# Kernel optimization log

Measured on AMD Instinct MI355X. Metric: run time of the kernel, lower is better.

## Reference

```python
import jax, jax.numpy as jnp
import numpy as np

MARGIN = 0.3
IN_FEATURES = 128
NUM_CLASSES = 100
BATCH = 4096


def setup_inputs() -> dict:
    key = jax.random.key(0)
    k1, k2, k3, k4 = jax.random.split(key, 4)
    embeddings = jax.random.normal(k1, (BATCH, IN_FEATURES), dtype=jnp.float32)
    labels = jax.random.randint(k2, (BATCH,), 0, NUM_CLASSES, dtype=jnp.int64)
    # nn.Linear params (kaiming-uniform-ish scale)
    bound = 1.0 / np.sqrt(IN_FEATURES)
    fc_w = jax.random.uniform(k3, (NUM_CLASSES, IN_FEATURES), jnp.float32, -bound, bound)
    fc_b = jax.random.uniform(k4, (NUM_CLASSES,), jnp.float32, -bound, bound)
    return {"embeddings": embeddings, "labels": labels, "fc_w": fc_w, "fc_b": fc_b}


def _triplet_hard(emb, labels, margin):
    # pairwise squared euclidean distances: ||a||^2 + ||b||^2 - 2 a.b
    sq = jnp.sum(emb * emb, axis=1)  # [B]
    d2 = sq[:, None] + sq[None, :] - 2.0 * (emb @ emb.T)
    dist = jnp.sqrt(jnp.clip(d2, 1e-12))  # [B, B]
    same = labels[:, None] == labels[None, :]  # [B, B] (diag True, as in torch)
    neg_inf = jnp.float32(-jnp.inf)
    pos_inf = jnp.float32(jnp.inf)
    ap = jnp.max(jnp.where(same, dist, neg_inf), axis=1)  # hardest positive
    an = jnp.min(jnp.where(same, pos_inf, dist), axis=1)  # hardest negative
    # MarginRankingLoss(target=1): mean(relu(-(an - ap) + margin))
    return jnp.mean(jax.nn.relu(ap - an + margin))


def _cross_entropy(logits, labels):
    logp = jax.nn.log_softmax(logits, axis=-1)
    return -jnp.mean(jnp.take_along_axis(logp, labels[:, None], axis=1)[:, 0])


def reference(embeddings, labels, fc_w, fc_b):
    logits = embeddings @ fc_w.T + fc_b  # [B, C]
    triplet = _triplet_hard(embeddings, labels, MARGIN)
    ce = _cross_entropy(logits, labels)
    return triplet + ce
```

## Files before the change

### kernel.cpp

```cpp
#include <hip/hip_runtime.h>
#include <math.h>

#define BATCH 4096
#define DIM 128
#define NCLS 100
#define MARGIN 0.3f

typedef __attribute__((ext_vector_type(8))) short short8;
typedef __attribute__((ext_vector_type(4))) float f32x4;

__device__ __forceinline__ unsigned short f2bf(float f) {
    unsigned int u = __float_as_uint(f);
    unsigned int r = (u + 0x7FFFu + ((u >> 16) & 1u)) >> 16;
    return (unsigned short)r;
}
__device__ __forceinline__ float bf2f(unsigned short b) {
    return __uint_as_float(((unsigned int)b) << 16);
}

__global__ __launch_bounds__(256) void prep_kernel(
        const float* __restrict__ emb, const float* __restrict__ fcw,
        unsigned short* __restrict__ ebf, float* __restrict__ sq,
        unsigned short* __restrict__ wbf) {
    int bid = blockIdx.x, tid = threadIdx.x;
    if (bid < 256) {
        int wave = tid >> 6, lane = tid & 63;
        #pragma unroll
        for (int r = 0; r < 4; ++r) {
            int row = bid * 16 + wave * 4 + r;
            const float2* src = reinterpret_cast<const float2*>(emb + row * DIM);
            float2 xy = src[lane];
            unsigned short b0 = f2bf(xy.x), b1 = f2bf(xy.y);
            float y0 = bf2f(b0), y1 = bf2f(b1);
            reinterpret_cast<unsigned int*>(ebf + row * DIM)[lane] =
                ((unsigned int)b1 << 16) | (unsigned int)b0;
            float acc = y0 * y0 + y1 * y1;
            #pragma unroll
            for (int off = 1; off < 64; off <<= 1) acc += __shfl_xor(acc, off, 64);
            if (lane == 0) sq[row] = acc;
        }
    } else {
        int idx = (bid - 256) * 256 + tid;
        for (int k = idx; k < 112 * DIM; k += 512) {
            wbf[k] = (k < NCLS * DIM) ? f2bf(fcw[k]) : (unsigned short)0;
        }
    }
}

__global__ __launch_bounds__(256) void main_kernel(
        const unsigned short* __restrict__ ebf, const unsigned short* __restrict__ wbf,
        const float* __restrict__ sq, const int* __restrict__ labels,
        const float* __restrict__ fcb,
        float* __restrict__ appart, float* __restrict__ anpart,
        float* __restrict__ ce) {
    __shared__ float lg[16][128];
    int bid = blockIdx.x, tid = threadIdx.x;
    int wave = tid >> 6, lane = tid & 63;
    int lm = lane & 15, lq = lane >> 4;
    int koff = lq * 8;

    if (bid < 1024) {
        int rowgrp = bid >> 4, chunk = bid & 15;
        int rbase = rowgrp * 64 + wave * 16;
        int arow = rbase + lm;
        const unsigned short* apt = ebf + arow * DIM + koff;
        short8 a0 = *reinterpret_cast<const short8*>(apt);
        short8 a1 = *reinterpret_cast<const short8*>(apt + 32);
        short8 a2 = *reinterpret_cast<const short8*>(apt + 64);
        short8 a3 = *reinterpret_cast<const short8*>(apt + 96);

        int labr[4];
        #pragma unroll
        for (int r = 0; r < 4; ++r) labr[r] = labels[rbase + lq * 4 + r];

        float rmax[4] = {-INFINITY, -INFINITY, -INFINITY, -INFINITY};
        float rmin[4] = { INFINITY,  INFINITY,  INFINITY,  INFINITY};

        int cbase = chunk * 256;
        #pragma unroll 4
        for (int ct = 0; ct < 16; ++ct) {
            int col = cbase + ct * 16 + lm;
            const unsigned short* bp = ebf + col * DIM + koff;
            short8 b0 = *reinterpret_cast<const short8*>(bp);
            short8 b1 = *reinterpret_cast<const short8*>(bp + 32);
            short8 b2 = *reinterpret_cast<const short8*>(bp + 64);
            short8 b3 = *reinterpret_cast<const short8*>(bp + 96);
            f32x4 c = {0.f, 0.f, 0.f, 0.f};
            c = __builtin_amdgcn_mfma_f32_16x16x32_bf16(a0, b0, c, 0, 0, 0);
            c = __builtin_amdgcn_mfma_f32_16x16x32_bf16(a1, b1, c, 0, 0, 0);
            c = __builtin_amdgcn_mfma_f32_16x16x32_bf16(a2, b2, c, 0, 0, 0);
            c = __builtin_amdgcn_mfma_f32_16x16x32_bf16(a3, b3, c, 0, 0, 0);
            float sqc = sq[col];
            int lc = labels[col];
            #pragma unroll
            for (int r = 0; r < 4; ++r) {
                float v = fmaf(c[r], -2.0f, sqc);
                bool same = (lc == labr[r]);
                rmax[r] = same ? fmaxf(rmax[r], v) : rmax[r];
                rmin[r] = same ? rmin[r] : fminf(rmin[r], v);
            }
        }
        #pragma unroll
        for (int off = 1; off < 16; off <<= 1) {
            #pragma unroll
            for (int r = 0; r < 4; ++r) {
                rmax[r] = fmaxf(rmax[r], __shfl_xor(rmax[r], off, 64));
                rmin[r] = fminf(rmin[r], __shfl_xor(rmin[r], off, 64));
            }
        }
        if (lm == 0) {
            int row0 = rbase + lq * 4;
            #pragma unroll
            for (int r = 0; r < 4; ++r) {
                appart[(row0 + r) * 16 + chunk] = rmax[r];
                anpart[(row0 + r) * 16 + chunk] = rmin[r];
            }
        }
    } else {
        int R0 = (bid - 1024) * 16;
        lg[tid >> 4][112 + (tid & 15)] = -INFINITY;

        int arow = R0 + lm;
        const unsigned short* apt = ebf + arow * DIM + koff;
        short8 a0 = *reinterpret_cast<const short8*>(apt);
        short8 a1 = *reinterpret_cast<const short8*>(apt + 32);
        short8 a2 = *reinterpret_cast<const short8*>(apt + 64);
        short8 a3 = *reinterpret_cast<const short8*>(apt + 96);

        for (int t = wave * 2; t < 7 && t < wave * 2 + 2; ++t) {
            int cls = t * 16 + lm;
            const unsigned short* bp = wbf + cls * DIM + koff;
            short8 b0 = *reinterpret_cast<const short8*>(bp);
            short8 b1 = *reinterpret_cast<const short8*>(bp + 32);
            short8 b2 = *reinterpret_cast<const short8*>(bp + 64);
            short8 b3 = *reinterpret_cast<const short8*>(bp + 96);
            f32x4 c = {0.f, 0.f, 0.f, 0.f};
            c = __builtin_amdgcn_mfma_f32_16x16x32_bf16(a0, b0, c, 0, 0, 0);
            c = __builtin_amdgcn_mfma_f32_16x16x32_bf16(a1, b1, c, 0, 0, 0);
            c = __builtin_amdgcn_mfma_f32_16x16x32_bf16(a2, b2, c, 0, 0, 0);
            c = __builtin_amdgcn_mfma_f32_16x16x32_bf16(a3, b3, c, 0, 0, 0);
            float bias = (cls < NCLS) ? fcb[cls] : -INFINITY;
            #pragma unroll
            for (int r = 0; r < 4; ++r)
                lg[lq * 4 + r][t * 16 + lm] = c[r] + bias;
        }
        __syncthreads();
        #pragma unroll
        for (int i = 0; i < 4; ++i) {
            int r = wave * 4 + i;
            float x0 = lg[r][lane], x1 = lg[r][lane + 64];
            float m = fmaxf(x0, x1);
            #pragma unroll
            for (int off = 1; off < 64; off <<= 1) m = fmaxf(m, __shfl_xor(m, off, 64));
            float s = expf(x0 - m) + expf(x1 - m);
            #pragma unroll
            for (int off = 1; off < 64; off <<= 1) s += __shfl_xor(s, off, 64);
            if (lane == 0) {
                int lab = labels[R0 + r];
                ce[R0 + r] = (m + logf(s)) - lg[r][lab];
            }
        }
    }
}

__global__ __launch_bounds__(256) void final_kernel(
        const float* __restrict__ sq, const float* __restrict__ appart,
        const float* __restrict__ anpart, const float* __restrict__ ce,
        float* __restrict__ out) {
    __shared__ float red[256];
    int tid = threadIdx.x, bid = blockIdx.x;
    float acc = 0.f;
    #pragma unroll
    for (int rr = 0; rr < 2; ++rr) {
        int row = bid * 512 + rr * 256 + tid;
        const float4* ap = reinterpret_cast<const float4*>(appart + row * 16);
        const float4* an = reinterpret_cast<const float4*>(anpart + row * 16);
        float m = -INFINITY, n = INFINITY;
        #pragma unroll
        for (int p = 0; p < 4; ++p) {
            float4 a = ap[p];
            m = fmaxf(m, fmaxf(fmaxf(a.x, a.y), fmaxf(a.z, a.w)));
            float4 b = an[p];
            n = fminf(n, fminf(fminf(b.x, b.y), fminf(b.z, b.w)));
        }
        float api = sqrtf(fmaxf(sq[row] + m, 1e-12f));
        float ani = sqrtf(fmaxf(sq[row] + n, 1e-12f));
        acc += fmaxf(api - ani + MARGIN, 0.f) + ce[row];
    }
    red[tid] = acc;
    __syncthreads();
    for (int s = 128; s > 0; s >>= 1) {
        if (tid < s) red[tid] += red[tid + s];
        __syncthreads();
    }
    if (tid == 0) atomicAdd(out, red[0] * (1.0f / BATCH));
}

extern "C" void kernel_launch(void* const* d_in, const int* in_sizes, int n_in,
                              void* d_out, int out_size, void* d_ws, size_t ws_size,
                              hipStream_t stream) {
    const float* emb    = (const float*)d_in[0];
    const int*   labels = (const int*)  d_in[1];
    const float* fcw    = (const float*)d_in[2];
    const float* fcb    = (const float*)d_in[3];
    float* out = (float*)d_out;

    char* ws = (char*)d_ws;
    unsigned short* ebf = (unsigned short*)(ws);
    unsigned short* wbf = (unsigned short*)(ws + 1048576);
    float* sq     = (float*)(ws + 1081344);
    float* ce     = (float*)(ws + 1097728);
    float* appart = (float*)(ws + 1114112);
    float* anpart = (float*)(ws + 1376256);

    hipMemsetAsync(out, 0, sizeof(float), stream);
    prep_kernel<<<258, 256, 0, stream>>>(emb, fcw, ebf, sq, wbf);
    main_kernel<<<1280, 256, 0, stream>>>(ebf, wbf, sq, labels, fcb, appart, anpart, ce);
    final_kernel<<<8, 256, 0, stream>>>(sq, appart, anpart, ce, out);
}
```

Measured before the change: 109.2 us.

## Fuse final reduction into main kernel via last-block atomic ticket

Removes the separate final reduction kernel and the memset of the output. Each main-kernel block takes an atomic ticket after a threadfence, and the last block to finish does the full reduction over all 4096 rows and writes the output directly. The ticket is reset in the prep kernel. This saves two launches/stream operations, but the tail reduction now runs serially in a single block instead of eight.

```diff
diff --git a/kernel.cpp b/kernel.cpp
--- a/kernel.cpp
+++ b/kernel.cpp
@@ -5,6 +5,7 @@
 #define DIM 128
 #define NCLS 100
 #define MARGIN 0.3f
+#define GRID_MAIN 1280
 
 typedef __attribute__((ext_vector_type(8))) short short8;
 typedef __attribute__((ext_vector_type(4))) float f32x4;
@@ -21,7 +22,7 @@
 __global__ __launch_bounds__(256) void prep_kernel(
         const float* __restrict__ emb, const float* __restrict__ fcw,
         unsigned short* __restrict__ ebf, float* __restrict__ sq,
-        unsigned short* __restrict__ wbf) {
+        unsigned short* __restrict__ wbf, int* __restrict__ ticket) {
     int bid = blockIdx.x, tid = threadIdx.x;
     if (bid < 256) {
         int wave = tid >> 6, lane = tid & 63;
@@ -40,6 +41,7 @@
             if (lane == 0) sq[row] = acc;
         }
     } else {
+        if (bid == 256 && tid == 0) *ticket = 0;
         int idx = (bid - 256) * 256 + tid;
         for (int k = idx; k < 112 * DIM; k += 512) {
             wbf[k] = (k < NCLS * DIM) ? f2bf(fcw[k]) : (unsigned short)0;
@@ -52,8 +54,10 @@
         const float* __restrict__ sq, const int* __restrict__ labels,
         const float* __restrict__ fcb,
         float* __restrict__ appart, float* __restrict__ anpart,
-        float* __restrict__ ce) {
+        float* __restrict__ ce, int* __restrict__ ticket,
+        float* __restrict__ out) {
     __shared__ float lg[16][128];
+    __shared__ int lastFlag;
     int bid = blockIdx.x, tid = threadIdx.x;
     int wave = tid >> 6, lane = tid & 63;
     int lm = lane & 15, lq = lane >> 4;
@@ -161,39 +165,40 @@
             }
         }
     }
-}
-
-__global__ __launch_bounds__(256) void final_kernel(
-        const float* __restrict__ sq, const float* __restrict__ appart,
-        const float* __restrict__ anpart, const float* __restrict__ ce,
-        float* __restrict__ out) {
-    __shared__ float red[256];
-    int tid = threadIdx.x, bid = blockIdx.x;
-    float acc = 0.f;
-    #pragma unroll
-    for (int rr = 0; rr < 2; ++rr) {
-        int row = bid * 512 + rr * 256 + tid;
-        const float4* ap = reinterpret_cast<const float4*>(appart + row * 16);
-        const float4* an = reinterpret_cast<const float4*>(anpart + row * 16);
-        float m = -INFINITY, n = INFINITY;
-        #pragma unroll
-        for (int p = 0; p < 4; ++p) {
-            float4 a = ap[p];
-            m = fmaxf(m, fmaxf(fmaxf(a.x, a.y), fmaxf(a.z, a.w)));
-            float4 b = an[p];
-            n = fminf(n, fminf(fminf(b.x, b.y), fminf(b.z, b.w)));
-        }
-        float api = sqrtf(fmaxf(sq[row] + m, 1e-12f));
-        float ani = sqrtf(fmaxf(sq[row] + n, 1e-12f));
-        acc += fmaxf(api - ani + MARGIN, 0.f) + ce[row];
+
+    __threadfence();
+    __syncthreads();
+    if (tid == 0) lastFlag = (atomicAdd(ticket, 1) == GRID_MAIN - 1);
+    __syncthreads();
+    if (lastFlag) {
+        __threadfence();
+        float acc = 0.f;
+        #pragma unroll
+        for (int rr = 0; rr < 16; ++rr) {
+            int row = rr * 256 + tid;
+            const float4* ap = reinterpret_cast<const float4*>(appart + row * 16);
+            const float4* an = reinterpret_cast<const float4*>(anpart + row * 16);
+            float m = -INFINITY, n = INFINITY;
+            #pragma unroll
+            for (int p = 0; p < 4; ++p) {
+                float4 a = ap[p];
+                m = fmaxf(m, fmaxf(fmaxf(a.x, a.y), fmaxf(a.z, a.w)));
+                float4 b = an[p];
+                n = fminf(n, fminf(fminf(b.x, b.y), fminf(b.z, b.w)));
+            }
+            float api = sqrtf(fmaxf(sq[row] + m, 1e-12f));
+            float ani = sqrtf(fmaxf(sq[row] + n, 1e-12f));
+            acc += fmaxf(api - ani + MARGIN, 0.f) + ce[row];
+        }
+        float* red = reinterpret_cast<float*>(lg);
+        red[tid] = acc;
+        __syncthreads();
+        for (int s = 128; s > 0; s >>= 1) {
+            if (tid < s) red[tid] += red[tid + s];
+            __syncthreads();
+        }
+        if (tid == 0) out[0] = red[0] * (1.0f / BATCH);
     }
-    red[tid] = acc;
-    __syncthreads();
-    for (int s = 128; s > 0; s >>= 1) {
-        if (tid < s) red[tid] += red[tid + s];
-        __syncthreads();
-    }
-    if (tid == 0) atomicAdd(out, red[0] * (1.0f / BATCH));
 }
 
 extern "C" void kernel_launch(void* const* d_in, const int* in_sizes, int n_in,
@@ -212,9 +217,9 @@
     float* ce     = (float*)(ws + 1097728);
     float* appart = (float*)(ws + 1114112);
     float* anpart = (float*)(ws + 1376256);
-
-    hipMemsetAsync(out, 0, sizeof(float), stream);
-    prep_kernel<<<258, 256, 0, stream>>>(emb, fcw, ebf, sq, wbf);
-    main_kernel<<<1280, 256, 0, stream>>>(ebf, wbf, sq, labels, fcb, appart, anpart, ce);
-    final_kernel<<<8, 256, 0, stream>>>(sq, appart, anpart, ce, out);
-}
+    int*   ticket = (int*)  (ws + 1638400);
+
+    prep_kernel<<<258, 256, 0, stream>>>(emb, fcw, ebf, sq, wbf, ticket);
+    main_kernel<<<GRID_MAIN, 256, 0, stream>>>(ebf, wbf, sq, labels, fcb,
+                                               appart, anpart, ce, ticket, out);
+}
```

Result: slower. 225.6 us (+106.6%).
